# Kernel optimization log

Measured on AMD Instinct MI355X. Metric: run time of the kernel, lower is better.

The kernel has to match this reference:

```python
import jax, jax.numpy as jnp
import numpy as np

N = 20000      # nodes
E = 256000     # edges
ESM = 1280     # esm_dim
H = 4          # heads
C = 256        # hidden_dim (per-head out)
HC = H * C     # 1024, concat width


def setup_inputs() -> dict:
    key = jax.random.key(0)
    ks = jax.random.split(key, 12)
    s = 0.02
    x = jax.random.normal(ks[0], (N, ESM), jnp.float32)
    edge_index = jax.random.randint(ks[1], (2, E), 0, N, dtype=jnp.int32)
    edge_weights = jax.random.uniform(ks[2], (E,), jnp.float32)
    # GATv2Conv params (PyG): lin_l (src, bias), lin_r (dst, no bias), lin_edge (no bias), att, out bias
    Wl = jax.random.normal(ks[3], (ESM, HC), jnp.float32) * s
    bl = jnp.zeros((HC,), jnp.float32)
    Wr = jax.random.normal(ks[4], (ESM, HC), jnp.float32) * s
    We = jax.random.normal(ks[5], (1, HC), jnp.float32) * s
    att = jax.random.normal(ks[6], (H, C), jnp.float32) * s
    b_gat = jnp.zeros((HC,), jnp.float32)
    # SAGEConv params: lin_l on mean-aggregated neighbors (bias), lin_r on root (no bias)
    Wsl = jax.random.normal(ks[7], (HC, ESM), jnp.float32) * s
    bsl = jnp.zeros((ESM,), jnp.float32)
    Wsr = jax.random.normal(ks[8], (HC, ESM), jnp.float32) * s
    # LayerNorm
    gamma = jnp.ones((ESM,), jnp.float32)
    beta = jnp.zeros((ESM,), jnp.float32)
    return dict(x=x, edge_index=edge_index, edge_weights=edge_weights,
                Wl=Wl, bl=bl, Wr=Wr, We=We, att=att, b_gat=b_gat,
                Wsl=Wsl, bsl=bsl, Wsr=Wsr, gamma=gamma, beta=beta)


def reference(x, edge_index, edge_weights, Wl, bl, Wr, We, att, b_gat,
              Wsl, bsl, Wsr, gamma, beta):
    src, dst = edge_index[0], edge_index[1]
    ew = edge_weights[:, None]                                    # [E,1]
    ones = jnp.ones((E,), x.dtype)
    deg = jax.ops.segment_sum(ones, dst, num_segments=N)          # in-degree [N]
    # ---- GATv2: add self-loops, edge_attr fill_value='mean' (mean of incoming attrs)
    loop_attr = jax.ops.segment_sum(ew, dst, num_segments=N) / jnp.maximum(deg, 1.0)[:, None]
    loop = jnp.arange(N, dtype=src.dtype)
    src_f = jnp.concatenate([src, loop])
    dst_f = jnp.concatenate([dst, loop])
    ea = jnp.concatenate([ew, loop_attr], axis=0)                 # [E+N,1]
    xl = (x @ Wl + bl).reshape(N, H, C)                           # source transform
    xr = (x @ Wr).reshape(N, H, C)                                # target transform
    ee = (ea @ We).reshape(-1, H, C)                              # edge transform
    m = jax.nn.leaky_relu(xl[src_f] + xr[dst_f] + ee, 0.2)        # [E+N,H,C]
    logits = jnp.einsum('ehc,hc->eh', m, att)                     # [E+N,H]
    amax = jax.ops.segment_max(logits, dst_f, num_segments=N)
    ex = jnp.exp(logits - amax[dst_f])
    den = jax.ops.segment_sum(ex, dst_f, num_segments=N)
    alpha = ex / (den[dst_f] + 1e-16)                             # softmax per dst node
    gat = jax.ops.segment_sum(alpha[:, :, None] * xl[src_f], dst_f, num_segments=N)
    gat = gat.reshape(N, HC) + b_gat
    h = jax.nn.elu(gat)
    # ---- SAGEConv: mean neighbor aggregation (no self loops) + root weight
    agg = jax.ops.segment_sum(h[src], dst, num_segments=N) / jnp.maximum(deg, 1.0)[:, None]
    y = jax.nn.relu(agg @ Wsl + bsl + h @ Wsr)
    # ---- residual + LayerNorm
    z = y + x
    mu = jnp.mean(z, axis=-1, keepdims=True)
    var = jnp.mean(jnp.square(z - mu), axis=-1, keepdims=True)
    return (z - mu) * jax.lax.rsqrt(var + 1e-5) * gamma + beta
```

## Files before the change

### kernel.cpp

```cpp
#include <hip/hip_runtime.h>
#include <hip/hip_bf16.h>
#include <math.h>

constexpr int kN   = 20000;
constexpr int kE   = 256000;
constexpr int kESM = 1280;
constexpr int kHC  = 1024;

typedef unsigned int  u32;
typedef unsigned short ushort_t;
typedef __bf16 bf16x8 __attribute__((ext_vector_type(8)));
typedef float  f32x4  __attribute__((ext_vector_type(4)));
typedef unsigned short u16x8 __attribute__((ext_vector_type(8)));
typedef unsigned short u16x4 __attribute__((ext_vector_type(4)));
typedef __attribute__((address_space(1))) const u32 gu32;
typedef __attribute__((address_space(3))) u32 lu32;

static __device__ __forceinline__ unsigned short f2bf_rne(float f) {
    u32 u = __float_as_uint(f);
    u32 r = (u + 0x7FFFu + ((u >> 16) & 1u)) >> 16;
    return (unsigned short)r;
}
static __device__ __forceinline__ float bf2f(unsigned short h) {
    return __uint_as_float(((u32)h) << 16);
}

__global__ __launch_bounds__(256) void deg_kernel(
    const int* __restrict__ dst, const float* __restrict__ ew,
    int* __restrict__ deg, float* __restrict__ wsum)
{
    int e = blockIdx.x * 256 + threadIdx.x;
    if (e < kE) {
        int d = dst[e];
        atomicAdd(&deg[d], 1);
        atomicAdd(&wsum[d], ew[e]);
    }
}

__global__ __launch_bounds__(1024) void scan_kernel(
    const int* __restrict__ deg, float* __restrict__ loopat,
    int* __restrict__ offsets)
{
    __shared__ int wsum[16];
    const int tid = threadIdx.x, wave = tid >> 6, lane = tid & 63;
    int base = 0;
    if (tid == 0) offsets[0] = 0;
    for (int t0 = 0; t0 < kN; t0 += 1024) {
        const int i = t0 + tid;
        int d = (i < kN) ? deg[i] : 0;
        if (i < kN) loopat[i] = loopat[i] / fmaxf((float)d, 1.0f);
        int v = d;
#pragma unroll
        for (int off = 1; off < 64; off <<= 1) {
            int u = __shfl_up(v, off, 64);
            if (lane >= off) v += u;
        }
        if (lane == 63) wsum[wave] = v;
        __syncthreads();
        if (wave == 0) {
            int s = (lane < 16) ? wsum[lane] : 0;
#pragma unroll
            for (int off = 1; off < 16; off <<= 1) {
                int u = __shfl_up(s, off, 64);
                if (lane >= off) s += u;
            }
            if (lane < 16) wsum[lane] = s;
        }
        __syncthreads();
        const int prefix = base + (wave ? wsum[wave - 1] : 0);
        if (i < kN) offsets[i + 1] = prefix + v;
        base += wsum[15];
        __syncthreads();
    }
}

__global__ __launch_bounds__(256) void sort_kernel(
    const int* __restrict__ src, const int* __restrict__ dst,
    const float* __restrict__ ew, const int* __restrict__ offsets,
    int* __restrict__ cnt, int* __restrict__ ssrc, float* __restrict__ sew)
{
    int e = blockIdx.x * 256 + threadIdx.x;
    if (e < kE) {
        int d = dst[e];
        int p = offsets[d] + atomicAdd(&cnt[d], 1);
        ssrc[p] = src[e];
        sew[p]  = ew[e];
    }
}


__global__ __launch_bounds__(512) void pack_a_kernel(
    const float* __restrict__ A, int M, int K,
    int NKB, ushort_t* __restrict__ dst)
{
    const int kb = blockIdx.x, mb = blockIdx.y;
    const int tid = threadIdx.x;
    const int g = tid >> 7, r = tid & 127;
    const int row = mb * 128 + r;

    u16x8 hi, lo;
    if (row < M) {
        const float* src = A + (size_t)row * K + kb * 32 + g * 8;
        float4 v0 = *(const float4*)src;
        float4 v1 = *(const float4*)(src + 4);
        float vals[8] = {v0.x, v0.y, v0.z, v0.w, v1.x, v1.y, v1.z, v1.w};
#pragma unroll
        for (int j = 0; j < 8; ++j) {
            unsigned short h = f2bf_rne(vals[j]);
            hi[j] = h;
            lo[j] = f2bf_rne(vals[j] - bf2f(h));
        }
    } else {
#pragma unroll
        for (int j = 0; j < 8; ++j) { hi[j] = 0; lo[j] = 0; }
    }
    ushort_t* tb = dst + ((size_t)mb * NKB + kb) * 8192;
    *(u16x8*)&tb[0    + g * 1024 + r * 8] = hi;
    *(u16x8*)&tb[4096 + g * 1024 + r * 8] = lo;
}

constexpr size_t kA2Blk = 393216;
__global__ __launch_bounds__(512) void pack_a2_kernel(
    const float* __restrict__ agg, const ushort_t* __restrict__ hb,
    int M, ushort_t* __restrict__ dst)
{
    const int kb = blockIdx.x, mb = blockIdx.y;
    const int tid = threadIdx.x;
    const int g = tid >> 7, r = tid & 127;
    const int row = mb * 128 + r;

    if (kb < 32) {
        ushort_t* tb = dst + (size_t)mb * kA2Blk + (size_t)kb * 8192;
        u16x8 hi, lo;
        if (row < M) {
            const float* src = agg + (size_t)row * 1024 + kb * 32 + g * 8;
            float4 v0 = *(const float4*)src;
            float4 v1 = *(const float4*)(src + 4);
            float vals[8] = {v0.x, v0.y, v0.z, v0.w, v1.x, v1.y, v1.z, v1.w};
#pragma unroll
            for (int j = 0; j < 8; ++j) {
                unsigned short h = f2bf_rne(vals[j]);
                hi[j] = h;
                lo[j] = f2bf_rne(vals[j] - bf2f(h));
            }
        } else {
#pragma unroll
            for (int j = 0; j < 8; ++j) { hi[j] = 0; lo[j] = 0; }
        }
        *(u16x8*)&tb[0    + g * 1024 + r * 8] = hi;
        *(u16x8*)&tb[4096 + g * 1024 + r * 8] = lo;
    } else {
        ushort_t* tb = dst + (size_t)mb * kA2Blk + 262144 + (size_t)(kb - 32) * 4096;
        u16x8 hi;
        if (row < M) {
            hi = *(const u16x8*)&hb[(size_t)row * 1024 + (kb - 32) * 32 + g * 8];
        } else {
#pragma unroll
            for (int j = 0; j < 8; ++j) hi[j] = 0;
        }
        *(u16x8*)&tb[g * 1024 + r * 8] = hi;
    }
}

__global__ __launch_bounds__(512) void pack_b_kernel(
    const float* __restrict__ B1, const float* __restrict__ B2,
    int N, int split, int mode, ushort_t* __restrict__ dst)
{
    const int kb = blockIdx.x, nb = blockIdx.y;
    const int NKB = gridDim.x;
    const int tid = threadIdx.x;
    const int g = tid >> 7, c = tid & 127;
    const int n = nb * 128 + c;

    u16x8 hi, lo;
#pragma unroll
    for (int j = 0; j < 8; ++j) {
        int k = kb * 32 + g * 8 + j;
        float v;
        if (mode == 0) {
            v = (n < split) ? B1[(size_t)k * split + n]
                            : B2[(size_t)k * (N - split) + (n - split)];
        } else {
            v = (k < split) ? B1[(size_t)k * N + n]
                            : B2[(size_t)(k - split) * N + n];
        }
        unsigned short h = f2bf_rne(v);
        hi[j] = h;
        lo[j] = f2bf_rne(v - bf2f(h));
    }
    ushort_t* tb = dst + ((size_t)nb * NKB + kb) * 8192;
    *(u16x8*)&tb[0    + g * 1024 + c * 8] = hi;
    *(u16x8*)&tb[4096 + g * 1024 + c * 8] = lo;
}

__global__ __launch_bounds__(256) void gemm_mfma(
    const ushort_t* __restrict__ Ap, const ushort_t* __restrict__ Bp,
    const float* __restrict__ bias, int biasN,
    const float* __restrict__ resid, float* __restrict__ C,
    ushort_t* __restrict__ Cbf,
    int M, int N, int NKB, int nkb_full, int do_relu)
{
    __shared__ ushort_t sb[16384];
    const int tid  = threadIdx.x;
    const int wid  = tid >> 6;
    const int lane = tid & 63;
    const int l15 = lane & 15, l4 = lane >> 4;

    const int nwg = gridDim.x * gridDim.y;
    const int lin = blockIdx.y * gridDim.x + blockIdx.x;
    const int q = nwg >> 3, r = nwg & 7;
    const int xcd = lin & 7, pos = lin >> 3;
    const int swz = (xcd < r ? xcd * (q + 1) : r * (q + 1) + (xcd - r) * q) + pos;
    const int mb = swz / gridDim.x, nb = swz % gridDim.x;
    const int wr = wid >> 1, wc = wid & 1;

    f32x4 acc[4][4];
#pragma unroll
    for (int i = 0; i < 4; ++i)
#pragma unroll
        for (int j = 0; j < 4; ++j) acc[i][j] = (f32x4){0.f, 0.f, 0.f, 0.f};

    const size_t a_blk = (size_t)nkb_full * 8192 + (size_t)(NKB - nkb_full) * 4096;
    const char* at = (const char*)(Ap + (size_t)mb * a_blk);
    const char* bt = (const char*)(Bp + (size_t)nb * NKB * 8192);

    for (int kb = 0; kb < nkb_full; ++kb) {
        const char* atk = at + (size_t)kb * 16384;
        const char* btk = bt + (size_t)kb * 16384;
#pragma unroll
        for (int c = 0; c < 4; ++c) {
            __builtin_amdgcn_global_load_lds(
                (gu32*)(atk + c * 4096 + tid * 16),
                (lu32*)&sb[c * 2048 + wid * 512], 16, 0, 0);
            __builtin_amdgcn_global_load_lds(
                (gu32*)(btk + c * 4096 + tid * 16),
                (lu32*)&sb[8192 + c * 2048 + wid * 512], 16, 0, 0);
        }
        __syncthreads();

        bf16x8 af[2][4], bv[2][4];
#pragma unroll
        for (int hl = 0; hl < 2; ++hl)
#pragma unroll
            for (int m = 0; m < 4; ++m)
                af[hl][m] = *(const bf16x8*)&sb[hl * 4096 + l4 * 1024 + (wr * 64 + m * 16 + l15) * 8];
#pragma unroll
        for (int hl = 0; hl < 2; ++hl)
#pragma unroll
            for (int n = 0; n < 4; ++n)
                bv[hl][n] = *(const bf16x8*)&sb[8192 + hl * 4096 + l4 * 1024 + (wc * 64 + n * 16 + l15) * 8];

#pragma unroll
        for (int m = 0; m < 4; ++m)
#pragma unroll
            for (int n = 0; n < 4; ++n) {
                acc[m][n] = __builtin_amdgcn_mfma_f32_16x16x32_bf16(af[0][m], bv[0][n], acc[m][n], 0, 0, 0);
                acc[m][n] = __builtin_amdgcn_mfma_f32_16x16x32_bf16(af[0][m], bv[1][n], acc[m][n], 0, 0, 0);
                acc[m][n] = __builtin_amdgcn_mfma_f32_16x16x32_bf16(af[1][m], bv[0][n], acc[m][n], 0, 0, 0);
            }
        __syncthreads();
    }

    for (int kb = nkb_full; kb < NKB; ++kb) {
        const char* atk = at + (size_t)nkb_full * 16384 + (size_t)(kb - nkb_full) * 8192;
        const char* btk = bt + (size_t)kb * 16384;
#pragma unroll
        for (int c = 0; c < 2; ++c) {
            __builtin_amdgcn_global_load_lds(
                (gu32*)(atk + c * 4096 + tid * 16),
                (lu32*)&sb[c * 2048 + wid * 512], 16, 0, 0);
        }
#pragma unroll
        for (int c = 0; c < 4; ++c) {
            __builtin_amdgcn_global_load_lds(
                (gu32*)(btk + c * 4096 + tid * 16),
                (lu32*)&sb[8192 + c * 2048 + wid * 512], 16, 0, 0);
        }
        __syncthreads();

        bf16x8 af0[4], bv[2][4];
#pragma unroll
        for (int m = 0; m < 4; ++m)
            af0[m] = *(const bf16x8*)&sb[l4 * 1024 + (wr * 64 + m * 16 + l15) * 8];
#pragma unroll
        for (int hl = 0; hl < 2; ++hl)
#pragma unroll
            for (int n = 0; n < 4; ++n)
                bv[hl][n] = *(const bf16x8*)&sb[8192 + hl * 4096 + l4 * 1024 + (wc * 64 + n * 16 + l15) * 8];

#pragma unroll
        for (int m = 0; m < 4; ++m)
#pragma unroll
            for (int n = 0; n < 4; ++n) {
                acc[m][n] = __builtin_amdgcn_mfma_f32_16x16x32_bf16(af0[m], bv[0][n], acc[m][n], 0, 0, 0);
                acc[m][n] = __builtin_amdgcn_mfma_f32_16x16x32_bf16(af0[m], bv[1][n], acc[m][n], 0, 0, 0);
            }
        __syncthreads();
    }

    const int row_w = mb * 128 + wr * 64;
    const int col_w = nb * 128 + wc * 64;
    if (Cbf) {
        const bool isxl = (col_w < 1024);
#pragma unroll
        for (int m = 0; m < 4; ++m) {
#pragma unroll
            for (int n = 0; n < 4; ++n) {
                const int col = col_w + n * 16 + l15;
#pragma unroll
                for (int j = 0; j < 4; ++j) {
                    const int row = row_w + m * 16 + l4 * 4 + j;
                    if (row < M) {
                        float v = acc[m][n][j];
                        if (isxl) {
                            v += bias[col];
                            Cbf[(size_t)row * 1024 + col] = f2bf_rne(v);
                        } else {
                            C[(size_t)row * 1024 + (col - 1024)] = v;
                        }
                    }
                }
            }
        }
    } else {
#pragma unroll
        for (int m = 0; m < 4; ++m) {
#pragma unroll
            for (int n = 0; n < 4; ++n) {
                const int col = col_w + n * 16 + l15;
#pragma unroll
                for (int j = 0; j < 4; ++j) {
                    const int row = row_w + m * 16 + l4 * 4 + j;
                    if (row < M) {
                        float v = acc[m][n][j];
                        if (bias && col < biasN) v += bias[col];
                        if (do_relu) v = fmaxf(v, 0.f);
                        if (resid) v += resid[(size_t)row * N + col];
                        C[(size_t)row * N + col] = v;
                    }
                }
            }
        }
    }
}

__global__ __launch_bounds__(256) void gat2_kernel(
    const ushort_t* __restrict__ xlb, const float* __restrict__ xrb,
    const int* __restrict__ ssrc, const float* __restrict__ sew,
    const int* __restrict__ offsets, const float* __restrict__ loopat,
    const float* __restrict__ We, const float* __restrict__ att,
    const float* __restrict__ bgat, ushort_t* __restrict__ hout)
{
    const int n = blockIdx.x;
    const int base = threadIdx.x * 4;

    const float4 xr4 = *(const float4*)&xrb[(size_t)n * 1024 + base];
    const float4 We4 = *(const float4*)&We[base];
    const float4 at4 = *(const float4*)&att[base];

    float M = -INFINITY, D = 0.f;
    float4 acc = make_float4(0.f, 0.f, 0.f, 0.f);

    const int beg = offsets[n], end = offsets[n + 1];
    for (int e = beg; e <= end; ++e) {
        int s; float w;
        if (e < end) { s = ssrc[e]; w = sew[e]; }
        else         { s = n;       w = loopat[n]; }

        const u16x4 xh = *(const u16x4*)&xlb[(size_t)s * 1024 + base];
        float4 xls;
        xls.x = bf2f(xh[0]); xls.y = bf2f(xh[1]);
        xls.z = bf2f(xh[2]); xls.w = bf2f(xh[3]);
        float m0 = xls.x + xr4.x + w * We4.x;
        float m1 = xls.y + xr4.y + w * We4.y;
        float m2 = xls.z + xr4.z + w * We4.z;
        float m3 = xls.w + xr4.w + w * We4.w;
        m0 = (m0 >= 0.f) ? m0 : 0.2f * m0;
        m1 = (m1 >= 0.f) ? m1 : 0.2f * m1;
        m2 = (m2 >= 0.f) ? m2 : 0.2f * m2;
        m3 = (m3 >= 0.f) ? m3 : 0.2f * m3;
        float p = m0 * at4.x + m1 * at4.y + m2 * at4.z + m3 * at4.w;
#pragma unroll
        for (int o = 32; o >= 1; o >>= 1) p += __shfl_xor(p, o, 64);

        float newM  = fmaxf(M, p);
        float scale = __expf(M - newM);
        float wexp  = __expf(p - newM);
        D     = D * scale + wexp;
        acc.x = acc.x * scale + wexp * xls.x;
        acc.y = acc.y * scale + wexp * xls.y;
        acc.z = acc.z * scale + wexp * xls.z;
        acc.w = acc.w * scale + wexp * xls.w;
        M = newM;
    }

    const float inv = 1.0f / (D + 1e-16f);
    float g0 = acc.x * inv + bgat[base + 0];
    float g1 = acc.y * inv + bgat[base + 1];
    float g2 = acc.z * inv + bgat[base + 2];
    float g3 = acc.w * inv + bgat[base + 3];
    u16x4 hv;
    hv[0] = f2bf_rne((g0 > 0.f) ? g0 : expm1f(g0));
    hv[1] = f2bf_rne((g1 > 0.f) ? g1 : expm1f(g1));
    hv[2] = f2bf_rne((g2 > 0.f) ? g2 : expm1f(g2));
    hv[3] = f2bf_rne((g3 > 0.f) ? g3 : expm1f(g3));
    *(u16x4*)&hout[(size_t)n * 1024 + base] = hv;
}

__global__ __launch_bounds__(256) void agg2_kernel(
    const ushort_t* __restrict__ hb, const int* __restrict__ ssrc,
    const int* __restrict__ offsets, float* __restrict__ aggout)
{
    const int n = blockIdx.x;
    const int base = threadIdx.x * 4;
    float4 a = make_float4(0.f, 0.f, 0.f, 0.f);
    const int beg = offsets[n], end = offsets[n + 1];
    for (int e = beg; e < end; ++e) {
        const u16x4 hv = *(const u16x4*)&hb[(size_t)ssrc[e] * 1024 + base];
        a.x += bf2f(hv[0]); a.y += bf2f(hv[1]);
        a.z += bf2f(hv[2]); a.w += bf2f(hv[3]);
    }
    const float inv = 1.0f / fmaxf((float)(end - beg), 1.0f);
    a.x *= inv; a.y *= inv; a.z *= inv; a.w *= inv;
    *(float4*)&aggout[(size_t)n * 1024 + base] = a;
}

__global__ __launch_bounds__(320) void ln_kernel(
    float* __restrict__ z, const float* __restrict__ gamma,
    const float* __restrict__ beta)
{
    const int r = blockIdx.x;
    const int t = threadIdx.x;
    const int wave = t >> 6, lane = t & 63;
    __shared__ float red[5];

    float4 v = *(const float4*)&z[(size_t)r * kESM + t * 4];
    float s = v.x + v.y + v.z + v.w;
#pragma unroll
    for (int o = 32; o >= 1; o >>= 1) s += __shfl_xor(s, o, 64);
    if (lane == 0) red[wave] = s;
    __syncthreads();
    s = red[0] + red[1] + red[2] + red[3] + red[4];
    const float mu = s * (1.0f / (float)kESM);

    float dx = v.x - mu, dy = v.y - mu, dz = v.z - mu, dw = v.w - mu;
    float q = dx * dx + dy * dy + dz * dz + dw * dw;
#pragma unroll
    for (int o = 32; o >= 1; o >>= 1) q += __shfl_xor(q, o, 64);
    __syncthreads();
    if (lane == 0) red[wave] = q;
    __syncthreads();
    q = red[0] + red[1] + red[2] + red[3] + red[4];
    const float rstd = rsqrtf(q * (1.0f / (float)kESM) + 1e-5f);

    const float4 g4 = *(const float4*)&gamma[t * 4];
    const float4 b4 = *(const float4*)&beta[t * 4];
    float4 o;
    o.x = dx * rstd * g4.x + b4.x;
    o.y = dy * rstd * g4.y + b4.y;
    o.z = dz * rstd * g4.z + b4.z;
    o.w = dw * rstd * g4.w + b4.w;
    *(float4*)&z[(size_t)r * kESM + t * 4] = o;
}

#define BM 128
#define BN 128
#define BK 16

__global__ __launch_bounds__(256) void gemm_kernel(
    const float* __restrict__ A,  const float* __restrict__ B,
    const float* __restrict__ A2, const float* __restrict__ B2,
    const float* __restrict__ bias, const float* __restrict__ resid,
    float* __restrict__ C, int M, int N, int K, int do_relu)
{
    __shared__ float As[BK][BM];
    __shared__ float Bs[BK][BN];

    const int tid = threadIdx.x;
    const int bm = blockIdx.y, bn = blockIdx.x;
    const int row0 = bm * BM, col0 = bn * BN;
    const int tx = tid & 15, ty = tid >> 4;

    float acc[8][8];
#pragma unroll
    for (int i = 0; i < 8; ++i)
#pragma unroll
        for (int j = 0; j < 8; ++j) acc[i][j] = 0.0f;

    const int arow  = tid >> 1;
    const int akoff = (tid & 1) * 8;
    const int bkr   = tid >> 4;
    const int bcol  = (tid & 15) * 8;

    for (int pair = 0; pair < 2; ++pair) {
        const float* Ap = pair ? A2 : A;
        const float* Bp = pair ? B2 : B;
        if (!Ap) break;
        for (int k0 = 0; k0 < K; k0 += BK) {
            float4 a0 = make_float4(0.f, 0.f, 0.f, 0.f);
            float4 a1 = a0;
            int gr = row0 + arow;
            if (gr < M) {
                const float* aptr = Ap + (size_t)gr * K + k0 + akoff;
                a0 = *(const float4*)aptr;
                a1 = *(const float4*)(aptr + 4);
            }
            const float* bptr = Bp + (size_t)(k0 + bkr) * N + col0 + bcol;
            float4 b0 = *(const float4*)bptr;
            float4 b1 = *(const float4*)(bptr + 4);

            __syncthreads();
            As[akoff + 0][arow] = a0.x;
            As[akoff + 1][arow] = a0.y;
            As[akoff + 2][arow] = a0.z;
            As[akoff + 3][arow] = a0.w;
            As[akoff + 4][arow] = a1.x;
            As[akoff + 5][arow] = a1.y;
            As[akoff + 6][arow] = a1.z;
            As[akoff + 7][arow] = a1.w;
            *(float4*)&Bs[bkr][bcol]     = b0;
            *(float4*)&Bs[bkr][bcol + 4] = b1;
            __syncthreads();

#pragma unroll
            for (int kk = 0; kk < BK; ++kk) {
                float4 a0r = *(const float4*)&As[kk][ty * 8];
                float4 a1r = *(const float4*)&As[kk][ty * 8 + 4];
                float4 b0r = *(const float4*)&Bs[kk][tx * 4];
                float4 b1r = *(const float4*)&Bs[kk][64 + tx * 4];
                float ar[8] = {a0r.x, a0r.y, a0r.z, a0r.w, a1r.x, a1r.y, a1r.z, a1r.w};
                float br[8] = {b0r.x, b0r.y, b0r.z, b0r.w, b1r.x, b1r.y, b1r.z, b1r.w};
#pragma unroll
                for (int i = 0; i < 8; ++i)
#pragma unroll
                    for (int j = 0; j < 8; ++j)
                        acc[i][j] = fmaf(ar[i], br[j], acc[i][j]);
            }
        }
    }

#pragma unroll
    for (int i = 0; i < 8; ++i) {
        int gr = row0 + ty * 8 + i;
        if (gr >= M) break;
#pragma unroll
        for (int half = 0; half < 2; ++half) {
            int gc = col0 + half * 64 + tx * 4;
            float4 out;
            float* o = &out.x;
            const float* rrow = resid ? (resid + (size_t)gr * N + gc) : nullptr;
#pragma unroll
            for (int j = 0; j < 4; ++j) {
                float v = acc[i][half * 4 + j];
                if (bias) v += bias[gc + j];
                if (do_relu) v = fmaxf(v, 0.0f);
                if (rrow) v += rrow[j];
                o[j] = v;
            }
            *(float4*)&C[(size_t)gr * N + gc] = out;
        }
    }
}

__global__ __launch_bounds__(256) void gat_kernel(
    const float* __restrict__ xl, const float* __restrict__ xr,
    const int* __restrict__ ssrc, const float* __restrict__ sew,
    const int* __restrict__ offsets, const float* __restrict__ loopat,
    const float* __restrict__ We, const float* __restrict__ att,
    const float* __restrict__ bgat, float* __restrict__ hout)
{
    const int n = blockIdx.x;
    const int base = threadIdx.x * 4;

    const float4 xr4 = *(const float4*)&xr[(size_t)n * kHC + base];
    const float4 We4 = *(const float4*)&We[base];
    const float4 at4 = *(const float4*)&att[base];

    float M = -INFINITY, D = 0.f;
    float4 acc = make_float4(0.f, 0.f, 0.f, 0.f);

    const int beg = offsets[n], end = offsets[n + 1];
    for (int e = beg; e <= end; ++e) {
        int s; float w;
        if (e < end) { s = ssrc[e]; w = sew[e]; }
        else         { s = n;       w = loopat[n]; }

        const float4 xls = *(const float4*)&xl[(size_t)s * kHC + base];
        float m0 = xls.x + xr4.x + w * We4.x;
        float m1 = xls.y + xr4.y + w * We4.y;
        float m2 = xls.z + xr4.z + w * We4.z;
        float m3 = xls.w + xr4.w + w * We4.w;
        m0 = (m0 >= 0.f) ? m0 : 0.2f * m0;
        m1 = (m1 >= 0.f) ? m1 : 0.2f * m1;
        m2 = (m2 >= 0.f) ? m2 : 0.2f * m2;
        m3 = (m3 >= 0.f) ? m3 : 0.2f * m3;
        float p = m0 * at4.x + m1 * at4.y + m2 * at4.z + m3 * at4.w;
#pragma unroll
        for (int o = 32; o >= 1; o >>= 1) p += __shfl_xor(p, o, 64);

        float newM  = fmaxf(M, p);
        float scale = __expf(M - newM);
        float wexp  = __expf(p - newM);
        D     = D * scale + wexp;
        acc.x = acc.x * scale + wexp * xls.x;
        acc.y = acc.y * scale + wexp * xls.y;
        acc.z = acc.z * scale + wexp * xls.z;
        acc.w = acc.w * scale + wexp * xls.w;
        M = newM;
    }

    const float inv = 1.0f / (D + 1e-16f);
    float g0 = acc.x * inv + bgat[base + 0];
    float g1 = acc.y * inv + bgat[base + 1];
    float g2 = acc.z * inv + bgat[base + 2];
    float g3 = acc.w * inv + bgat[base + 3];
    float4 hv;
    hv.x = (g0 > 0.f) ? g0 : expm1f(g0);
    hv.y = (g1 > 0.f) ? g1 : expm1f(g1);
    hv.z = (g2 > 0.f) ? g2 : expm1f(g2);
    hv.w = (g3 > 0.f) ? g3 : expm1f(g3);
    *(float4*)&hout[(size_t)n * kHC + base] = hv;
}

__global__ __launch_bounds__(256) void agg_kernel(
    const float* __restrict__ h, const int* __restrict__ ssrc,
    const int* __restrict__ offsets, float* __restrict__ aggout)
{
    const int n = blockIdx.x;
    const int base = threadIdx.x * 4;
    float4 a = make_float4(0.f, 0.f, 0.f, 0.f);
    const int beg = offsets[n], end = offsets[n + 1];
    for (int e = beg; e < end; ++e) {
        const float4 hv = *(const float4*)&h[(size_t)ssrc[e] * kHC + base];
        a.x += hv.x; a.y += hv.y; a.z += hv.z; a.w += hv.w;
    }
    const float inv = 1.0f / fmaxf((float)(end - beg), 1.0f);
    a.x *= inv; a.y *= inv; a.z *= inv; a.w *= inv;
    *(float4*)&aggout[(size_t)n * kHC + base] = a;
}

__global__ __launch_bounds__(256) void scan_kernel_fb(
    const int* __restrict__ deg, float* __restrict__ loopat,
    int* __restrict__ offsets)
{
    __shared__ int s[256];
    int tid = threadIdx.x;
    int base = 0;
    if (tid == 0) offsets[0] = 0;
    for (int t0 = 0; t0 < kN; t0 += 256) {
        int i = t0 + tid;
        int d = (i < kN) ? deg[i] : 0;
        if (i < kN) {
            float w = loopat[i];
            loopat[i] = w / fmaxf((float)d, 1.0f);
        }
        s[tid] = d;
        int v = d;
        for (int off = 1; off < 256; off <<= 1) {
            __syncthreads();
            int add = (tid >= off) ? s[tid - off] : 0;
            __syncthreads();
            v += add;
            s[tid] = v;
        }
        __syncthreads();
        if (i < kN) offsets[i + 1] = base + v;
        base += s[255];
        __syncthreads();
    }
}

extern "C" void kernel_launch(void* const* d_in, const int* in_sizes, int n_in,
                              void* d_out, int out_size, void* d_ws, size_t ws_size,
                              hipStream_t stream)
{
    const float* x     = (const float*)d_in[0];
    const int*   ei    = (const int*)  d_in[1];
    const float* ew    = (const float*)d_in[2];
    const float* Wl    = (const float*)d_in[3];
    const float* bl    = (const float*)d_in[4];
    const float* Wr    = (const float*)d_in[5];
    const float* We    = (const float*)d_in[6];
    const float* att   = (const float*)d_in[7];
    const float* bgat  = (const float*)d_in[8];
    const float* Wsl   = (const float*)d_in[9];
    const float* bsl   = (const float*)d_in[10];
    const float* Wsr   = (const float*)d_in[11];
    const float* gamma = (const float*)d_in[12];
    const float* beta  = (const float*)d_in[13];
    const int* src = ei;
    const int* dst = ei + kE;
    char* ws = (char*)d_ws;

    const size_t SZ_XLB  = (size_t)kN * 1024 * 2;
    const size_t SZ_XRB  = (size_t)kN * 1024 * 4;
    const size_t SZ_B1   = (size_t)16 * 40 * 16384;
    const size_t SZ_XPK  = (size_t)157 * 40 * 16384;
    const size_t SZ_HBF  = (size_t)kN * 1024 * 2;
    const size_t SZ_B2   = (size_t)10 * 64 * 16384;
    const size_t OFF_XRB = SZ_XLB;
    const size_t OFF_B1  = OFF_XRB + SZ_XRB;
    const size_t OFF_XPK = OFF_B1 + SZ_B1;
    const size_t OFF_HBF = OFF_XPK + SZ_XPK;
    const size_t OFF_B2  = OFF_HBF + SZ_HBF;
    size_t off = OFF_B2 + SZ_B2;
    auto salloc = [&](size_t bytes) -> void* {
        void* p = ws + off;
        off = (off + bytes + 255) & ~(size_t)255;
        return p;
    };
    int*   deg    = (int*)  salloc((size_t)kN * 4);
    int*   cnt    = (int*)  salloc((size_t)kN * 4);
    int*   offs   = (int*)  salloc((size_t)(kN + 1) * 4);
    float* loopat = (float*)salloc((size_t)kN * 4);
    int*   ssrc   = (int*)  salloc((size_t)kE * 4);
    float* sew    = (float*)salloc((size_t)kE * 4);
    const size_t FAST_TOTAL = off;

    if (ws_size >= FAST_TOTAL) {
        ushort_t* xlb   = (ushort_t*)(ws);
        float*    xrb   = (float*)   (ws + OFF_XRB);
        ushort_t* b1p   = (ushort_t*)(ws + OFF_B1);
        ushort_t* xpack = (ushort_t*)(ws + OFF_XPK);
        ushort_t* hbuf  = (ushort_t*)(ws + OFF_HBF);
        ushort_t* b2p   = (ushort_t*)(ws + OFF_B2);
        float*    aggb  = (float*)   (ws + OFF_XPK);
        ushort_t* apack = (ushort_t*)(ws);

        hipMemsetAsync(deg,    0, (size_t)kN * 4, stream);
        hipMemsetAsync(cnt,    0, (size_t)kN * 4, stream);
        hipMemsetAsync(loopat, 0, (size_t)kN * 4, stream);

        deg_kernel <<<(kE + 255) / 256, 256, 0, stream>>>(dst, ew, deg, loopat);
        scan_kernel<<<1, 1024, 0, stream>>>(deg, loopat, offs);
        sort_kernel<<<(kE + 255) / 256, 256, 0, stream>>>(src, dst, ew, offs, cnt, ssrc, sew);

        pack_a_kernel<<<dim3(40, 157), 512, 0, stream>>>(x, kN, kESM, 40, xpack);
        pack_b_kernel<<<dim3(40, 16), 512, 0, stream>>>(Wl, Wr, 2048, 1024, 0, b1p);
        pack_b_kernel<<<dim3(64, 10), 512, 0, stream>>>(Wsl, Wsr, 1280, 1024, 1, b2p);

        gemm_mfma<<<dim3(16, 157), 256, 0, stream>>>(xpack, b1p, bl, 1024,
                                                     nullptr, xrb, xlb,
                                                     kN, 2048, 40, 40, 0);

        gat2_kernel<<<kN, 256, 0, stream>>>(xlb, xrb, ssrc, sew, offs, loopat,
                                            We, att, bgat, hbuf);
        agg2_kernel<<<kN, 256, 0, stream>>>(hbuf, ssrc, offs, aggb);

        pack_a2_kernel<<<dim3(64, 157), 512, 0, stream>>>(aggb, hbuf, kN, apack);

        gemm_mfma<<<dim3(10, 157), 256, 0, stream>>>(apack, b2p, bsl, 1280,
                                                     x, (float*)d_out, nullptr,
                                                     kN, 1280, 64, 32, 1);

        ln_kernel<<<kN, 320, 0, stream>>>((float*)d_out, gamma, beta);
    } else {
        size_t foff = 0;
        auto falloc = [&](size_t bytes) -> void* {
            void* p = ws + foff;
            foff = (foff + bytes + 255) & ~(size_t)255;
            return p;
        };
        int*   fdeg    = (int*)  falloc((size_t)kN * 4);
        int*   fcnt    = (int*)  falloc((size_t)kN * 4);
        int*   foffs   = (int*)  falloc((size_t)(kN + 1) * 4);
        float* floopat = (float*)falloc((size_t)kN * 4);
        int*   fssrc   = (int*)  falloc((size_t)kE * 4);
        float* fsew    = (float*)falloc((size_t)kE * 4);
        float* bufA    = (float*)falloc((size_t)kN * kHC * 4);
        float* bufB    = (float*)falloc((size_t)kN * kHC * 4);

        hipMemsetAsync(fdeg,    0, (size_t)kN * 4, stream);
        hipMemsetAsync(fcnt,    0, (size_t)kN * 4, stream);
        hipMemsetAsync(floopat, 0, (size_t)kN * 4, stream);

        deg_kernel <<<(kE + 255) / 256, 256, 0, stream>>>(dst, ew, fdeg, floopat);
        scan_kernel_fb<<<1, 256, 0, stream>>>(fdeg, floopat, foffs);
        sort_kernel<<<(kE + 255) / 256, 256, 0, stream>>>(src, dst, ew, foffs, fcnt, fssrc, fsew);

        dim3 g1(kHC / BN, (kN + BM - 1) / BM);
        gemm_kernel<<<g1, 256, 0, stream>>>(x, Wl, nullptr, nullptr, bl, nullptr,
                                            bufA, kN, kHC, kESM, 0);
        gemm_kernel<<<g1, 256, 0, stream>>>(x, Wr, nullptr, nullptr, nullptr, nullptr,
                                            bufB, kN, kHC, kESM, 0);

        gat_kernel<<<kN, 256, 0, stream>>>(bufA, bufB, fssrc, fsew, foffs, floopat,
                                           We, att, bgat, bufB);
        agg_kernel<<<kN, 256, 0, stream>>>(bufB, fssrc, foffs, bufA);

        dim3 g2(kESM / BN, (kN + BM - 1) / BM);
        gemm_kernel<<<g2, 256, 0, stream>>>(bufA, Wsl, bufB, Wsr, bsl, x,
                                            (float*)d_out, kN, kESM, kHC, 1);

        ln_kernel<<<kN, 320, 0, stream>>>((float*)d_out, gamma, beta);
    }
}
```

Before: 1.282 ms.

## Drop bf16 split-precision for x in GEMM1 and batch GAT softmax per chunk

The x packing now emits only the bf16 high part instead of a hi/lo pair, so the first GEMM runs fewer MFMA passes (the lo-term count argument becomes 0). The GATv2 kernel is restructured: each wave computes logits for different edges across all four heads, stores them in shared memory, and a chunked two-pass softmax (max, exp, weighted sum) replaces the per-edge serial online softmax with its per-edge shuffle reductions. The workspace layout is reshuffled to fit the smaller packed buffer. Dropping the lo term lowers accuracy of xl/xr, and the new GAT kernel reads each source row twice and adds block barriers.

After: 1.276 ms. No clear change (-0.5%).

```diff
diff --git a/kernel.cpp b/kernel.cpp
--- a/kernel.cpp
+++ b/kernel.cpp
@@ -98,25 +98,20 @@
     const int g = tid >> 7, r = tid & 127;
     const int row = mb * 128 + r;
 
-    u16x8 hi, lo;
+    u16x8 hi;
     if (row < M) {
         const float* src = A + (size_t)row * K + kb * 32 + g * 8;
         float4 v0 = *(const float4*)src;
         float4 v1 = *(const float4*)(src + 4);
         float vals[8] = {v0.x, v0.y, v0.z, v0.w, v1.x, v1.y, v1.z, v1.w};
 #pragma unroll
-        for (int j = 0; j < 8; ++j) {
-            unsigned short h = f2bf_rne(vals[j]);
-            hi[j] = h;
-            lo[j] = f2bf_rne(vals[j] - bf2f(h));
-        }
+        for (int j = 0; j < 8; ++j) hi[j] = f2bf_rne(vals[j]);
     } else {
 #pragma unroll
-        for (int j = 0; j < 8; ++j) { hi[j] = 0; lo[j] = 0; }
-    }
-    ushort_t* tb = dst + ((size_t)mb * NKB + kb) * 8192;
-    *(u16x8*)&tb[0    + g * 1024 + r * 8] = hi;
-    *(u16x8*)&tb[4096 + g * 1024 + r * 8] = lo;
+        for (int j = 0; j < 8; ++j) hi[j] = 0;
+    }
+    ushort_t* tb = dst + ((size_t)mb * NKB + kb) * 4096;
+    *(u16x8*)&tb[g * 1024 + r * 8] = hi;
 }
 
 constexpr size_t kA2Blk = 393216;
@@ -352,46 +347,93 @@
     const float* __restrict__ bgat, ushort_t* __restrict__ hout)
 {
     const int n = blockIdx.x;
-    const int base = threadIdx.x * 4;
-
-    const float4 xr4 = *(const float4*)&xrb[(size_t)n * 1024 + base];
-    const float4 We4 = *(const float4*)&We[base];
-    const float4 at4 = *(const float4*)&att[base];
-
-    float M = -INFINITY, D = 0.f;
+    const int tid = threadIdx.x;
+    const int wave = tid >> 6, lane = tid & 63;
+    __shared__ float slog[4][512];
+    __shared__ float sNewM[4];
+
+    float4 xr1[4], We1[4], at1[4];
+#pragma unroll
+    for (int i = 0; i < 4; ++i) {
+        const int c = i * 256 + lane * 4;
+        xr1[i] = *(const float4*)&xrb[(size_t)n * 1024 + c];
+        We1[i] = *(const float4*)&We[c];
+        at1[i] = *(const float4*)&att[c];
+    }
+
+    const int beg = offsets[n], end = offsets[n + 1];
+    const int base = tid * 4;
+
+    float Mloc = -INFINITY, D = 0.f;
     float4 acc = make_float4(0.f, 0.f, 0.f, 0.f);
 
-    const int beg = offsets[n], end = offsets[n + 1];
-    for (int e = beg; e <= end; ++e) {
-        int s; float w;
-        if (e < end) { s = ssrc[e]; w = sew[e]; }
-        else         { s = n;       w = loopat[n]; }
-
-        const u16x4 xh = *(const u16x4*)&xlb[(size_t)s * 1024 + base];
-        float4 xls;
-        xls.x = bf2f(xh[0]); xls.y = bf2f(xh[1]);
-        xls.z = bf2f(xh[2]); xls.w = bf2f(xh[3]);
-        float m0 = xls.x + xr4.x + w * We4.x;
-        float m1 = xls.y + xr4.y + w * We4.y;
-        float m2 = xls.z + xr4.z + w * We4.z;
-        float m3 = xls.w + xr4.w + w * We4.w;
-        m0 = (m0 >= 0.f) ? m0 : 0.2f * m0;
-        m1 = (m1 >= 0.f) ? m1 : 0.2f * m1;
-        m2 = (m2 >= 0.f) ? m2 : 0.2f * m2;
-        m3 = (m3 >= 0.f) ? m3 : 0.2f * m3;
-        float p = m0 * at4.x + m1 * at4.y + m2 * at4.z + m3 * at4.w;
-#pragma unroll
-        for (int o = 32; o >= 1; o >>= 1) p += __shfl_xor(p, o, 64);
-
-        float newM  = fmaxf(M, p);
-        float scale = __expf(M - newM);
-        float wexp  = __expf(p - newM);
-        D     = D * scale + wexp;
-        acc.x = acc.x * scale + wexp * xls.x;
-        acc.y = acc.y * scale + wexp * xls.y;
-        acc.z = acc.z * scale + wexp * xls.z;
-        acc.w = acc.w * scale + wexp * xls.w;
-        M = newM;
+    for (int cbeg = beg; cbeg <= end; cbeg += 512) {
+        const int cend = min(cbeg + 512, end + 1);
+        const int cn = cend - cbeg;
+
+        for (int e = cbeg + wave; e < cend; e += 4) {
+            int s; float w;
+            if (e < end) { s = ssrc[e]; w = sew[e]; }
+            else         { s = n;       w = loopat[n]; }
+            const ushort_t* xrow = &xlb[(size_t)s * 1024];
+            float p[4];
+#pragma unroll
+            for (int i = 0; i < 4; ++i) {
+                const int c = i * 256 + lane * 4;
+                const u16x4 xh = *(const u16x4*)&xrow[c];
+                float m0 = bf2f(xh[0]) + xr1[i].x + w * We1[i].x;
+                float m1 = bf2f(xh[1]) + xr1[i].y + w * We1[i].y;
+                float m2 = bf2f(xh[2]) + xr1[i].z + w * We1[i].z;
+                float m3 = bf2f(xh[3]) + xr1[i].w + w * We1[i].w;
+                m0 = (m0 >= 0.f) ? m0 : 0.2f * m0;
+                m1 = (m1 >= 0.f) ? m1 : 0.2f * m1;
+                m2 = (m2 >= 0.f) ? m2 : 0.2f * m2;
+                m3 = (m3 >= 0.f) ? m3 : 0.2f * m3;
+                p[i] = m0 * at1[i].x + m1 * at1[i].y + m2 * at1[i].z + m3 * at1[i].w;
+            }
+#pragma unroll
+            for (int i = 0; i < 4; ++i)
+#pragma unroll
+                for (int o = 32; o >= 1; o >>= 1) p[i] += __shfl_xor(p[i], o, 64);
+            if (lane == 0) {
+                const int idx = e - cbeg;
+                slog[0][idx] = p[0]; slog[1][idx] = p[1];
+                slog[2][idx] = p[2]; slog[3][idx] = p[3];
+            }
+        }
+        __syncthreads();
+
+        {
+            float m = Mloc;
+            for (int i = lane; i < cn; i += 64) m = fmaxf(m, slog[wave][i]);
+#pragma unroll
+            for (int o = 32; o >= 1; o >>= 1) m = fmaxf(m, __shfl_xor(m, o, 64));
+            if (lane == 0) sNewM[wave] = m;
+        }
+        __syncthreads();
+
+        for (int f = tid; f < 2048; f += 256) {
+            const int h = f >> 9, i = f & 511;
+            if (i < cn) slog[h][i] = __expf(slog[h][i] - sNewM[h]);
+        }
+        const float newM = sNewM[wave];
+        const float scale = __expf(Mloc - newM);
+        D *= scale;
+        acc.x *= scale; acc.y *= scale; acc.z *= scale; acc.w *= scale;
+        __syncthreads();
+
+        for (int e = cbeg; e < cend; ++e) {
+            const int s = (e < end) ? ssrc[e] : n;
+            const float wx = slog[wave][e - cbeg];
+            const u16x4 xh = *(const u16x4*)&xlb[(size_t)s * 1024 + base];
+            acc.x += wx * bf2f(xh[0]);
+            acc.y += wx * bf2f(xh[1]);
+            acc.z += wx * bf2f(xh[2]);
+            acc.w += wx * bf2f(xh[3]);
+            D += wx;
+        }
+        Mloc = newM;
+        __syncthreads();
     }
 
     const float inv = 1.0f / (D + 1e-16f);
@@ -694,16 +736,17 @@
 
     const size_t SZ_XLB  = (size_t)kN * 1024 * 2;
     const size_t SZ_XRB  = (size_t)kN * 1024 * 4;
-    const size_t SZ_B1   = (size_t)16 * 40 * 16384;
-    const size_t SZ_XPK  = (size_t)157 * 40 * 16384;
     const size_t SZ_HBF  = (size_t)kN * 1024 * 2;
     const size_t SZ_B2   = (size_t)10 * 64 * 16384;
+    const size_t SZ_APK  = (size_t)157 * kA2Blk * 2;
+    const size_t SZ_XPK  = (size_t)157 * 40 * 8192;
     const size_t OFF_XRB = SZ_XLB;
-    const size_t OFF_B1  = OFF_XRB + SZ_XRB;
-    const size_t OFF_XPK = OFF_B1 + SZ_B1;
-    const size_t OFF_HBF = OFF_XPK + SZ_XPK;
+    const size_t OFF_HBF = OFF_XRB + SZ_XRB;
     const size_t OFF_B2  = OFF_HBF + SZ_HBF;
-    size_t off = OFF_B2 + SZ_B2;
+    const size_t OFF_APK = OFF_B2 + SZ_B2;
+    const size_t OFF_XPK = OFF_APK;
+    const size_t OFF_B1  = OFF_APK + SZ_XPK;
+    size_t off = OFF_APK + SZ_APK;
     auto salloc = [&](size_t bytes) -> void* {
         void* p = ws + off;
         off = (off + bytes + 255) & ~(size_t)255;
@@ -720,12 +763,12 @@
     if (ws_size >= FAST_TOTAL) {
         ushort_t* xlb   = (ushort_t*)(ws);
         float*    xrb   = (float*)   (ws + OFF_XRB);
-        ushort_t* b1p   = (ushort_t*)(ws + OFF_B1);
-        ushort_t* xpack = (ushort_t*)(ws + OFF_XPK);
         ushort_t* hbuf  = (ushort_t*)(ws + OFF_HBF);
         ushort_t* b2p   = (ushort_t*)(ws + OFF_B2);
-        float*    aggb  = (float*)   (ws + OFF_XPK);
-        ushort_t* apack = (ushort_t*)(ws);
+        ushort_t* apack = (ushort_t*)(ws + OFF_APK);
+        ushort_t* xpack = (ushort_t*)(ws + OFF_XPK);
+        ushort_t* b1p   = (ushort_t*)(ws + OFF_B1);
+        float*    aggb  = (float*)   (ws);
 
         hipMemsetAsync(deg,    0, (size_t)kN * 4, stream);
         hipMemsetAsync(cnt,    0, (size_t)kN * 4, stream);
@@ -741,7 +784,7 @@
 
         gemm_mfma<<<dim3(16, 157), 256, 0, stream>>>(xpack, b1p, bl, 1024,
                                                      nullptr, xrb, xlb,
-                                                     kN, 2048, 40, 40, 0);
+                                                     kN, 2048, 40, 0, 0);
 
         gat2_kernel<<<kN, 256, 0, stream>>>(xlb, xrb, ssrc, sew, offs, loopat,
                                             We, att, bgat, hbuf);
```
